# Kernel optimization log

Hardware: AMD Instinct MI355X
Metric: run time of the kernel (lower is better)

## Reference

```python
import jax, jax.numpy as jnp
import numpy as np

OUT_K = 7  # out_kernel


def setup_inputs() -> dict:
    key = jax.random.key(0)
    k = jax.random.split(key, 12)
    b, cin, h, w = 2, 256, 64, 64
    C, pd = 64, 4          # out_channels, pos_dim
    qc = C - pd            # channels produced by conv_q/k/v
    s = 0.05
    f32 = jnp.float32
    return {
        "x":    jax.random.normal(k[0], (b, cin, h, w), f32),
        "Wq":   jax.random.normal(k[1], (qc, cin), f32) * s,
        "bq":   jax.random.normal(k[2], (qc,), f32) * s,
        "Wk":   jax.random.normal(k[3], (qc, cin), f32) * s,
        "bk":   jax.random.normal(k[4], (qc,), f32) * s,
        "Wv":   jax.random.normal(k[5], (qc, cin), f32) * s,
        "bv":   jax.random.normal(k[6], (qc,), f32) * s,
        "Wp":   jax.random.normal(k[7], (pd, 2), f32) * s,
        "bp":   jax.random.normal(k[8], (pd,), f32) * s,
        "Wout": jax.random.normal(k[9], (C, C, OUT_K, OUT_K), f32) * s,
        "bout": jax.random.normal(k[10], (C,), f32) * s,
    }


def reference(x, Wq, bq, Wk, bk, Wv, bv, Wp, bp, Wout, bout):
    b, cin, h, w = x.shape
    C = Wout.shape[0]  # out_channels
    dt = x.dtype

    # positional encoding: hw_pose is (row_index, col_index) grids -> 1x1 conv to pos_dim chans
    rows = jnp.broadcast_to(jnp.arange(h, dtype=dt)[:, None], (h, w))
    cols = jnp.broadcast_to(jnp.arange(w, dtype=dt)[None, :], (h, w))
    grid = jnp.stack([rows, cols], axis=0)                      # (2,h,w)
    pos = jnp.einsum('oc,chw->ohw', Wp, grid) + bp[:, None, None]  # (pd,h,w)
    pos = jnp.broadcast_to(pos[None], (b,) + pos.shape)         # (b,pd,h,w)

    def conv1x1(W, bias):
        return jnp.einsum('bchw,oc->bohw', x, W) + bias[None, :, None, None]

    qs = jnp.concatenate([conv1x1(Wq, bq), pos], axis=1)        # (b,C,h,w)
    ks = jnp.concatenate([conv1x1(Wk, bk), pos], axis=1)
    vs = jnp.concatenate([conv1x1(Wv, bv), pos], axis=1)

    hw = h * w
    qsf = qs.transpose(0, 2, 3, 1).reshape(b, hw, C)            # (b,hw,C)
    ksf = ks.reshape(b, C, hw)                                  # (b,C,hw)
    vsf = vs.transpose(0, 2, 3, 1)                              # (b,h,w,C)

    qk = jnp.einsum('bnc,bcm->bnm', qsf, ksf) / jnp.sqrt(jnp.asarray(C, dt))
    diag = jnp.arange(hw)
    qk = qk.at[:, diag, diag].set(0.0)                          # zero diagonal BEFORE softmax
    attn = jax.nn.softmax(qk, axis=-1).reshape(b, h, w, h, w)

    # 7x7 clamped neighborhood gather (replaces the 49-iteration python loop)
    r = OUT_K // 2
    offs = jnp.arange(-r, r + 1)
    hi = jnp.clip(jnp.arange(h)[:, None] + offs[None, :], 0, h - 1)  # (h,7)
    wi = jnp.clip(jnp.arange(w)[:, None] + offs[None, :], 0, w - 1)  # (w,7)
    ii = jnp.arange(h)[:, None, None, None]
    jj = jnp.arange(w)[None, :, None, None]
    hk = hi[:, None, :, None]
    wk = wi[None, :, None, :]
    attn_loc = attn[:, ii, jj, hk, wk]                          # (b,h,w,7,7)
    v_loc = vsf[:, hk, wk, :]                                   # (b,h,w,7,7,C)

    qkv = attn_loc[..., None] * v_loc                           # (b,h,w,7,7,C)
    # con_out: kernel=7, stride=7 over a 7x7 patch == full contraction
    out = jnp.einsum('bhwklc,ockl->bhwo', qkv, Wout) + bout     # (b,h,w,C)
    out = jax.nn.relu(out)
    return out.transpose(0, 3, 1, 2)                            # (b,C,h,w)
```

## Files before the change

### kernel.cpp

```cpp
#include <hip/hip_runtime.h>
#include <math.h>

#define NTAP 49

typedef short bf16x8 __attribute__((ext_vector_type(8)));
typedef float f32x4  __attribute__((ext_vector_type(4)));

__device__ __forceinline__ float b2f(ushort u) {
    return __uint_as_float(((unsigned)u) << 16);
}
__device__ __forceinline__ ushort f2b(float f) {
    unsigned u = __float_as_uint(f);
    return (ushort)((u + 0x7FFFu + ((u >> 16) & 1u)) >> 16);
}
__device__ __forceinline__ int iclamp(int x) { return min(max(x, 0), 63); }

#define LOG2E 1.44269504f
#define S2    (0.125f * LOG2E)

#define WTB_OFF 0u
#define QH_OFF  598016u
#define KH_OFF  1646592u
#define VH_OFF  2695168u
#define LP_OFF  3743744u
#define MXQ_OFF 4005888u
#define MXK_OFF 4006912u

__device__ __forceinline__ float mh_reduce(const float* __restrict__ MXq,
                                           const float* __restrict__ MXk,
                                           int b, int t, float* sh) {
    if (t < 64) {
        float a = fmaxf(MXq[(b << 7) + t], MXq[(b << 7) + 64 + t]);
        float k = fmaxf(MXk[(b << 7) + t], MXk[(b << 7) + 64 + t]);
        #pragma unroll
        for (int off = 1; off < 64; off <<= 1) {
            a = fmaxf(a, __shfl_xor(a, off, 64));
            k = fmaxf(k, __shfl_xor(k, off, 64));
        }
        if (t == 0) *sh = 0.125f * sqrtf(a) * sqrtf(k) + 1.0f;
    }
    __syncthreads();
    return *sh;
}

__global__ __launch_bounds__(512, 2) void k_qkv(
    const float* __restrict__ x,
    const float* __restrict__ Wq, const float* __restrict__ Wk, const float* __restrict__ Wv,
    const float* __restrict__ bq, const float* __restrict__ bk, const float* __restrict__ bv,
    const float* __restrict__ Wp, const float* __restrict__ bp,
    ushort* __restrict__ QKV, float* __restrict__ MXq, float* __restrict__ MXk)
{
    __shared__ ushort Xh[32 * 256];
    __shared__ ushort Xl[32 * 256];
    __shared__ ushort Wshl[192 * 64];
    __shared__ float  sqL[64];
    int bid0 = blockIdx.x;
    int bid  = (bid0 & 7) * 32 + (bid0 >> 3);
    int b   = bid >> 7;
    int n0  = (bid & 127) * 32;
    int t   = threadIdx.x;
    int w    = t >> 6;
    int L    = t & 63;
    int lrow = L & 15, lk = L >> 4;

    if (t < 64) sqL[t] = 0.f;
    {
        int p  = t & 31;
        int cg = t >> 5;
        #pragma unroll
        for (int it = 0; it < 2; ++it) {
            int cgi = cg + it * 16;
            float v[8];
            #pragma unroll
            for (int e = 0; e < 8; ++e)
                v[e] = x[((size_t)(b * 256 + cgi * 8 + e) << 12) + n0 + p];
            bf16x8 hi, lo;
            #pragma unroll
            for (int e = 0; e < 8; ++e) {
                ushort h = f2b(v[e]);
                hi[e] = (short)h;
                lo[e] = (short)f2b(v[e] - b2f(h));
            }
            int off = p * 256 + ((cgi * 8) ^ ((p & 7) * 8));
            *(bf16x8*)(Xh + off) = hi;
            *(bf16x8*)(Xl + off) = lo;
        }
    }

    int   s_och[3], s_g[3];
    bool  s_live[3];
    const float* s_src[3];
    #pragma unroll
    for (int s = 0; s < 3; ++s) {
        int g_idx = t + s * 512;
        int och = g_idx >> 3, g = g_idx & 7;
        int mat = och >> 6, o = och & 63;
        const float* Wm = (mat == 0) ? Wq : (mat == 1) ? Wk : Wv;
        s_och[s] = och; s_g[s] = g;
        s_live[s] = (o < 60);
        s_src[s] = Wm + o * 256 + (g & 3) * 8;
    }
    float4 wreg[3][2];

    #define ISSUE_W(c8) {                                                   \
        _Pragma("unroll")                                                   \
        for (int s = 0; s < 3; ++s) {                                       \
            if (s_live[s]) {                                                \
                const float* sp = s_src[s] + (c8) * 32;                     \
                wreg[s][0] = *(const float4*)(sp);                          \
                wreg[s][1] = *(const float4*)(sp + 4);                      \
            } else {                                                        \
                wreg[s][0] = make_float4(0.f,0.f,0.f,0.f);                  \
                wreg[s][1] = make_float4(0.f,0.f,0.f,0.f);                  \
            }                                                               \
        } }
    #define WRITE_W() {                                                     \
        _Pragma("unroll")                                                   \
        for (int s = 0; s < 3; ++s) {                                       \
            float vv[8] = {wreg[s][0].x, wreg[s][0].y, wreg[s][0].z,        \
                           wreg[s][0].w, wreg[s][1].x, wreg[s][1].y,        \
                           wreg[s][1].z, wreg[s][1].w};                     \
            bf16x8 val;                                                     \
            _Pragma("unroll")                                               \
            for (int e = 0; e < 8; ++e) {                                   \
                ushort h = f2b(vv[e]);                                      \
                val[e] = (s_g[s] < 4) ? (short)h                            \
                                      : (short)f2b(vv[e] - b2f(h));         \
            }                                                               \
            *(bf16x8*)((char*)Wshl + s_och[s] * 128 +                       \
                       ((s_g[s] * 16) ^ ((s_och[s] & 7) << 4))) = val;      \
        } }

    ISSUE_W(0);
    __syncthreads();
    WRITE_W();
    __syncthreads();

    int pxh = w >> 2;
    int ob  = (w & 3) * 48;
    int px  = pxh * 16 + lrow;

    f32x4 acc[3] = {{0,0,0,0},{0,0,0,0},{0,0,0,0}};

    for (int c8 = 0; c8 < 8; ++c8) {
        if (c8 + 1 < 8) ISSUE_W(c8 + 1);
        int cidx = (c8 * 4 + lk) * 8;
        int o0 = px * 256 + (cidx ^ ((px & 7) * 8));
        bf16x8 ah = *(const bf16x8*)(Xh + o0);
        bf16x8 al = *(const bf16x8*)(Xl + o0);
        __builtin_amdgcn_s_setprio(1);
        #pragma unroll
        for (int c = 0; c < 3; ++c) {
            int och = ob + c * 16 + lrow;
            const char* wb = (const char*)Wshl + och * 128;
            int swz = (och & 7) << 4;
            bf16x8 bh = *(const bf16x8*)(wb + ((lk * 16) ^ swz));
            bf16x8 bl = *(const bf16x8*)(wb + (((4 + lk) * 16) ^ swz));
            acc[c] = __builtin_amdgcn_mfma_f32_16x16x32_bf16(al, bh, acc[c], 0, 0, 0);
            acc[c] = __builtin_amdgcn_mfma_f32_16x16x32_bf16(ah, bl, acc[c], 0, 0, 0);
            acc[c] = __builtin_amdgcn_mfma_f32_16x16x32_bf16(ah, bh, acc[c], 0, 0, 0);
        }
        __builtin_amdgcn_s_setprio(0);
        __syncthreads();
        if (c8 + 1 < 8) WRITE_W();
        __syncthreads();
    }

    float s_q[4] = {0,0,0,0}, s_k[4] = {0,0,0,0};
    #pragma unroll
    for (int c = 0; c < 3; ++c) {
        int och = ob + c * 16 + lrow;
        int mat = och >> 6;
        int o   = och & 63;
        const float* bm = (mat == 0) ? bq : (mat == 1) ? bk : bv;
        ushort* Ob = QKV + (size_t)mat * 524288;
        if (o < 60) {
            float bias = bm[o];
            #pragma unroll
            for (int e = 0; e < 4; ++e) {
                int n = n0 + pxh * 16 + lk * 4 + e;
                float v = acc[c][e] + bias;
                Ob[((size_t)((b << 12) + n)) * 64 + o] = f2b(v);
                if (mat == 0) s_q[e] = fmaf(v, v, s_q[e]);
                else if (mat == 1) s_k[e] = fmaf(v, v, s_k[e]);
            }
        } else {
            int po = o - 60;
            float w0 = Wp[2 * po], w1 = Wp[2 * po + 1], b0 = bp[po];
            #pragma unroll
            for (int e = 0; e < 4; ++e) {
                int n = n0 + pxh * 16 + lk * 4 + e;
                float fi = (float)(n >> 6), fj = (float)(n & 63);
                float pv = fmaf(w0, fi, fmaf(w1, fj, b0));
                Ob[((size_t)((b << 12) + n)) * 64 + o] = f2b(pv);
                if (mat == 0) s_q[e] = fmaf(pv, pv, s_q[e]);
                else if (mat == 1) s_k[e] = fmaf(pv, pv, s_k[e]);
            }
        }
    }
    #pragma unroll
    for (int off = 1; off < 16; off <<= 1) {
        #pragma unroll
        for (int e = 0; e < 4; ++e) {
            s_q[e] += __shfl_xor(s_q[e], off, 64);
            s_k[e] += __shfl_xor(s_k[e], off, 64);
        }
    }
    if (lrow == 0) {
        #pragma unroll
        for (int e = 0; e < 4; ++e) {
            int pix = pxh * 16 + lk * 4 + e;
            atomicAdd(&sqL[pix],      s_q[e]);
            atomicAdd(&sqL[32 + pix], s_k[e]);
        }
    }
    __syncthreads();
    if (t < 32) {
        float q2 = sqL[t], k2 = sqL[32 + t];
        #pragma unroll
        for (int off = 1; off < 32; off <<= 1) {
            q2 = fmaxf(q2, __shfl_xor(q2, off, 64));
            k2 = fmaxf(k2, __shfl_xor(k2, off, 64));
        }
        if (t == 0) { MXq[bid] = q2; MXk[bid] = k2; }
    }
}

__global__ __launch_bounds__(512, 2) void k_stats(
    const float* __restrict__ Wout, ushort* __restrict__ Wtb,
    const ushort* __restrict__ QH, const ushort* __restrict__ KH,
    const float* __restrict__ MXq, const float* __restrict__ MXk,
    float* __restrict__ Lp)
{
    __shared__ ushort Ks[2][128 * 64];
    __shared__ float  mhs;
    int bid0 = blockIdx.x;
    int bid  = (bid0 & 7) * 64 + (bid0 >> 3);
    int ks  = bid & 7;
    int r   = bid >> 3;
    int b   = r >> 5;
    int n0  = (r & 31) * 128;
    int ck0 = ks * 512;
    int t = threadIdx.x;

    {
        int widx = bid * 512 + t;
        if (widx < 64 * 64 * NTAP) {
            int o   = widx / (64 * NTAP);
            int rem = widx - o * (64 * NTAP);
            int c   = rem / NTAP;
            int kl  = rem - c * NTAP;
            Wtb[(o * NTAP + kl) * 64 + c] = f2b(Wout[widx]);
        }
    }
    float bse = -mh_reduce(MXq, MXk, b, t, &mhs) * LOG2E;

    int w = t >> 6, L = t & 63;
    int lrow = L & 15, lk = L >> 4;

    size_t qbase = ((size_t)((b << 12) + n0 + w * 16 + lrow)) * 64 + lk * 8;
    bf16x8 a0 = *(const bf16x8*)(QH + qbase);
    bf16x8 a1 = *(const bf16x8*)(QH + qbase + 32);

    #pragma unroll
    for (int gi = 0; gi < 2; ++gi) {
        int g = t + gi * 512;
        int u = g >> 3, c8 = g & 7;
        bf16x8 val = *(const bf16x8*)(KH + ((size_t)((b << 12) + ck0 + u)) * 64 + c8 * 8);
        *(bf16x8*)((char*)Ks[0] + u * 128 + ((c8 * 16) ^ ((u & 7) << 4))) = val;
    }

    float rs0 = 0.f, rs1 = 0.f, rs2 = 0.f, rs3 = 0.f;

    for (int c = 0; c < 4; ++c) {
        bf16x8 st0, st1;
        int u0 = t >> 3, c80 = t & 7;
        int u1 = (t + 512) >> 3, c81 = t & 7;
        bool pf = (c + 1) < 4;
        if (pf) {
            st0 = *(const bf16x8*)(KH + ((size_t)((b << 12) + ck0 + (c + 1) * 128 + u0)) * 64 + c80 * 8);
            st1 = *(const bf16x8*)(KH + ((size_t)((b << 12) + ck0 + (c + 1) * 128 + u1)) * 64 + c81 * 8);
        }
        __syncthreads();
        const char* kb = (const char*)Ks[c & 1];
        __builtin_amdgcn_s_setprio(1);
        #pragma unroll
        for (int kg = 0; kg < 8; ++kg) {
            int u = kg * 16 + lrow;
            int swz = (u & 7) << 4;
            bf16x8 b0 = *(const bf16x8*)(kb + u * 128 + ((lk * 16) ^ swz));
            bf16x8 b1 = *(const bf16x8*)(kb + u * 128 + ((64 + lk * 16) ^ swz));
            f32x4 z = {0.f, 0.f, 0.f, 0.f};
            z = __builtin_amdgcn_mfma_f32_16x16x32_bf16(a0, b0, z, 0, 0, 0);
            z = __builtin_amdgcn_mfma_f32_16x16x32_bf16(a1, b1, z, 0, 0, 0);
            rs0 += exp2f(fmaf(z[0], S2, bse));
            rs1 += exp2f(fmaf(z[1], S2, bse));
            rs2 += exp2f(fmaf(z[2], S2, bse));
            rs3 += exp2f(fmaf(z[3], S2, bse));
        }
        __builtin_amdgcn_s_setprio(0);
        if (pf) {
            char* kn = (char*)Ks[(c + 1) & 1];
            *(bf16x8*)(kn + u0 * 128 + ((c80 * 16) ^ ((u0 & 7) << 4))) = st0;
            *(bf16x8*)(kn + u1 * 128 + ((c81 * 16) ^ ((u1 & 7) << 4))) = st1;
        }
    }
    #pragma unroll
    for (int off = 1; off < 16; off <<= 1) {
        rs0 += __shfl_xor(rs0, off, 64);
        rs1 += __shfl_xor(rs1, off, 64);
        rs2 += __shfl_xor(rs2, off, 64);
        rs3 += __shfl_xor(rs3, off, 64);
    }
    if (lrow == 0) {
        float* dst = Lp + ((size_t)(ks * 2 + b) << 12) + n0 + w * 16 + lk * 4;
        dst[0] = rs0; dst[1] = rs1; dst[2] = rs2; dst[3] = rs3;
    }
}

__global__ __launch_bounds__(512, 1) void k_out(
    const ushort* __restrict__ QH, const ushort* __restrict__ KH,
    const ushort* __restrict__ VH, const ushort* __restrict__ Wtb,
    const float* __restrict__ Lp,
    const float* __restrict__ MXq, const float* __restrict__ MXk,
    const float* __restrict__ bout, float* __restrict__ out)
{
    __shared__ ushort Vs[7 * 40 * 64];
    __shared__ ushort Kh[7 * 40 * 64];
    __shared__ ushort Ws[7 * 64 * 64];
    __shared__ float  Al2[NTAP * 36];
    __shared__ float  Lrow[32];
    __shared__ float  LcS[32];
    __shared__ float  mhs;
    int bid0 = blockIdx.x;
    int bid  = (bid0 & 7) * 32 + (bid0 >> 3);
    int b   = bid >> 7;
    int rem = bid & 127;
    int i   = rem >> 1;
    int j0  = (rem & 1) * 32;
    int n0  = (i << 6) + j0;
    int t   = threadIdx.x;
    int w    = t >> 6;
    int L    = t & 63;
    int lrow = L & 15, lk = L >> 4;

    float bse = -mh_reduce(MXq, MXk, b, t, &mhs) * LOG2E;
    float e0  = exp2f(bse);

    bf16x8 wreg[7];
    #define ISSUE_WS(kk) {                                                          \
        _Pragma("unroll")                                                           \
        for (int s = 0; s < 7; ++s) {                                               \
            int g = t + s * 512;                                                    \
            int c8 = g & 7, och = (g >> 3) & 63, ll = g >> 9;                       \
            wreg[s] = *(const bf16x8*)(Wtb + ((size_t)(och * NTAP + (kk) * 7 + ll)) * 64 + c8 * 8); \
        } }
    #define WRITE_WS() {                                                            \
        _Pragma("unroll")                                                           \
        for (int s = 0; s < 7; ++s) {                                               \
            int g = t + s * 512;                                                    \
            int c8 = g & 7, och = (g >> 3) & 63, ll = g >> 9;                       \
            *(bf16x8*)((char*)Ws + ll * 8192 + och * 128 +                          \
                       ((c8 * 16) ^ ((och & 7) << 4))) = wreg[s];                   \
        } }

    for (int g = t; g < 2 * 7 * 38 * 8; g += 512) {
        int which = g >= 7 * 38 * 8;
        int gg = which ? g - 7 * 38 * 8 : g;
        int kk = gg / 304;
        int r2 = gg - kk * 304;
        int u  = r2 >> 3, c8 = r2 & 7;
        int vr = iclamp(i + kk - 3);
        int vc = iclamp(j0 - 3 + u);
        const ushort* src = which ? KH : VH;
        ushort* dst = which ? Kh : Vs;
        bf16x8 val = *(const bf16x8*)(src + ((size_t)((b << 12) + (vr << 6) + vc)) * 64 + c8 * 8);
        *(bf16x8*)((char*)dst + kk * 5120 + u * 128 + ((c8 * 16) ^ ((u & 7) << 4))) = val;
    }
    ISSUE_WS(0);
    WRITE_WS();
    if (t < 32) {
        int n = n0 + t;
        float s = 0.f;
        #pragma unroll
        for (int ks = 0; ks < 8; ++ks)
            s += Lp[((size_t)(ks * 2 + b) << 12) + n];
        Lrow[t] = s;
    }
    __syncthreads();

    {
        int p = t >> 4, u = t & 15;
        int n = n0 + p;
        int pj = n & 63;
        const ushort* qr = QH + ((size_t)(b << 12) + n) * 64;
        bf16x8 qv[8];
        #pragma unroll
        for (int c8 = 0; c8 < 8; ++c8) qv[c8] = *(const bf16x8*)(qr + c8 * 8);

        int nt = (u == 0) ? 4 : 3;
        float d[4] = {0.f, 0.f, 0.f, 0.f};
        int srcs[4];
        const char* kbp[4];
        int swzs[4];
        #pragma unroll
        for (int m = 0; m < 4; ++m) {
            int tap = (m == 3) ? 48 : (u + 16 * m);
            int kk = tap / 7, ll = tap - kk * 7;
            srcs[m] = (iclamp(i + kk - 3) << 6) + iclamp(pj + ll - 3);
            int uu = p + ll;
            kbp[m]  = (const char*)Kh + kk * 5120 + uu * 128;
            swzs[m] = (uu & 7) << 4;
        }
        #pragma unroll
        for (int c8 = 0; c8 < 8; ++c8) {
            bf16x8 kv0 = *(const bf16x8*)(kbp[0] + ((c8 * 16) ^ swzs[0]));
            bf16x8 kv1 = *(const bf16x8*)(kbp[1] + ((c8 * 16) ^ swzs[1]));
            bf16x8 kv2 = *(const bf16x8*)(kbp[2] + ((c8 * 16) ^ swzs[2]));
            #pragma unroll
            for (int e = 0; e < 8; ++e) {
                float q = b2f((ushort)qv[c8][e]);
                d[0] = fmaf(q, b2f((ushort)kv0[e]), d[0]);
                d[1] = fmaf(q, b2f((ushort)kv1[e]), d[1]);
                d[2] = fmaf(q, b2f((ushort)kv2[e]), d[2]);
            }
        }
        if (nt == 4) {
            #pragma unroll
            for (int c8 = 0; c8 < 8; ++c8) {
                bf16x8 kv3 = *(const bf16x8*)(kbp[3] + ((c8 * 16) ^ swzs[3]));
                #pragma unroll
                for (int e = 0; e < 8; ++e)
                    d[3] = fmaf(b2f((ushort)qv[c8][e]), b2f((ushort)kv3[e]), d[3]);
            }
        }
        if (u == 8)
            LcS[p] = Lrow[p] - exp2f(fmaf(d[1], S2, bse)) + e0;
        __syncthreads();
        float rLc = 1.0f / LcS[p];
        for (int m = 0; m < nt; ++m) {
            int tap = (m == 3) ? 48 : (u + 16 * m);
            float A = (srcs[m] == n) ? (e0 * rLc)
                                     : (exp2f(fmaf(d[m], S2, bse)) * rLc);
            Al2[tap * 36 + p] = A;
        }
    }
    __syncthreads();

    int q16 = (w >> 2) << 4;
    int o16 = (w & 3) << 4;
    int oA  = o16 + lrow;
    int wswz = (oA & 7) << 4;
    f32x4 acc0 = {0.f, 0.f, 0.f, 0.f};

    for (int kk = 0; kk < 7; ++kk) {
        if (kk + 1 < 7) ISSUE_WS(kk + 1);
        const char* vrow = (const char*)Vs + kk * 5120;
        __builtin_amdgcn_s_setprio(1);
        #pragma unroll
        for (int ll = 0; ll < 7; ++ll) {
            int kl = kk * 7 + ll;
            int u = q16 + lrow + ll;
            const char* vb = vrow + u * 128;
            int swz = (u & 7) << 4;
            bf16x8 v0 = *(const bf16x8*)(vb + ((lk * 16) ^ swz));
            bf16x8 v1 = *(const bf16x8*)(vb + ((64 + lk * 16) ^ swz));
            float4 av = *(const float4*)(&Al2[kl * 36 + q16 + lk * 4]);
            const char* wb = (const char*)Ws + ll * 8192 + oA * 128;
            bf16x8 b00 = *(const bf16x8*)(wb + ((lk * 16) ^ wswz));
            bf16x8 b01 = *(const bf16x8*)(wb + (((4 + lk) * 16) ^ wswz));
            f32x4 z = {0.f, 0.f, 0.f, 0.f};
            z = __builtin_amdgcn_mfma_f32_16x16x32_bf16(v0, b00, z, 0, 0, 0);
            z = __builtin_amdgcn_mfma_f32_16x16x32_bf16(v1, b01, z, 0, 0, 0);
            acc0[0] = fmaf(av.x, z[0], acc0[0]);
            acc0[1] = fmaf(av.y, z[1], acc0[1]);
            acc0[2] = fmaf(av.z, z[2], acc0[2]);
            acc0[3] = fmaf(av.w, z[3], acc0[3]);
        }
        __builtin_amdgcn_s_setprio(0);
        __syncthreads();
        if (kk + 1 < 7) WRITE_WS();
        __syncthreads();
    }

    int o = oA;
    int nbase = n0 + q16 + lk * 4;
    float bb = bout[o];
    float4 v = make_float4(fmaxf(acc0[0] + bb, 0.f), fmaxf(acc0[1] + bb, 0.f),
                           fmaxf(acc0[2] + bb, 0.f), fmaxf(acc0[3] + bb, 0.f));
    *(float4*)(out + (((size_t)(b * 64 + o)) << 12) + nbase) = v;
}

extern "C" void kernel_launch(void* const* d_in, const int* in_sizes, int n_in,
                              void* d_out, int out_size, void* d_ws, size_t ws_size,
                              hipStream_t stream) {
    const float* x    = (const float*)d_in[0];
    const float* Wq   = (const float*)d_in[1];
    const float* bq   = (const float*)d_in[2];
    const float* Wk   = (const float*)d_in[3];
    const float* bk   = (const float*)d_in[4];
    const float* Wv   = (const float*)d_in[5];
    const float* bv   = (const float*)d_in[6];
    const float* Wp   = (const float*)d_in[7];
    const float* bp   = (const float*)d_in[8];
    const float* Wout = (const float*)d_in[9];
    const float* bout = (const float*)d_in[10];
    float* out = (float*)d_out;

    char* ws = (char*)d_ws;
    ushort* Wtb = (ushort*)(ws + WTB_OFF);
    ushort* QKV = (ushort*)(ws + QH_OFF);
    float*  Lp  = (float*)(ws + LP_OFF);
    float*  MXq = (float*)(ws + MXQ_OFF);
    float*  MXk = (float*)(ws + MXK_OFF);

    ushort* QH = QKV;
    ushort* KH = QKV + 524288;
    ushort* VH = QKV + 1048576;

    hipLaunchKernelGGL(k_qkv,   dim3(256), dim3(512), 0, stream,
                       x, Wq, Wk, Wv, bq, bk, bv, Wp, bp, QKV, MXq, MXk);
    hipLaunchKernelGGL(k_stats, dim3(512), dim3(512), 0, stream,
                       Wout, Wtb, QH, KH, MXq, MXk, Lp);
    hipLaunchKernelGGL(k_out,   dim3(256), dim3(512), 0, stream,
                       QH, KH, VH, Wtb, Lp, MXq, MXk, bout, out);
}
```

Baseline: 46.13 us.

## Double-buffer output-conv weight tiles in LDS, aliasing second buffer over K halo

Replaces the separate shared arrays with one manually laid-out LDS buffer so the 7x64x64 weight slice can be double-buffered. The second weight buffer reuses the K-halo region, which is dead after the attention-weight phase. With two buffers, the barrier before writing the next weight slice is dropped, leaving one barrier per kk iteration instead of two. The cost is a larger LDS footprint (about 157 KB) and reliance on the K region being unused by the time it is overwritten.

```diff
diff --git a/kernel.cpp b/kernel.cpp
--- a/kernel.cpp
+++ b/kernel.cpp
@@ -318,6 +318,14 @@
     }
 }
 
+#define SM_VS   0
+#define SM_WS0  35840
+#define SM_WS1  93184
+#define SM_KHA  93184
+#define SM_AL2  150528
+#define SM_LROW 157584
+#define SM_LCS  157712
+#define SM_MHS  157840
 __global__ __launch_bounds__(512, 1) void k_out(
     const ushort* __restrict__ QH, const ushort* __restrict__ KH,
     const ushort* __restrict__ VH, const ushort* __restrict__ Wtb,
@@ -325,13 +333,13 @@
     const float* __restrict__ MXq, const float* __restrict__ MXk,
     const float* __restrict__ bout, float* __restrict__ out)
 {
-    __shared__ ushort Vs[7 * 40 * 64];
-    __shared__ ushort Kh[7 * 40 * 64];
-    __shared__ ushort Ws[7 * 64 * 64];
-    __shared__ float  Al2[NTAP * 36];
-    __shared__ float  Lrow[32];
-    __shared__ float  LcS[32];
-    __shared__ float  mhs;
+    __shared__ __align__(16) char smem[157856];
+    char*  Vsb  = smem + SM_VS;
+    char*  Khb  = smem + SM_KHA;
+    float* Al2  = (float*)(smem + SM_AL2);
+    float* Lrow = (float*)(smem + SM_LROW);
+    float* LcS  = (float*)(smem + SM_LCS);
+
     int bid0 = blockIdx.x;
     int bid  = (bid0 & 7) * 32 + (bid0 >> 3);
     int b   = bid >> 7;
@@ -344,7 +352,7 @@
     int L    = t & 63;
     int lrow = L & 15, lk = L >> 4;
 
-    float bse = -mh_reduce(MXq, MXk, b, t, &mhs) * LOG2E;
+    float bse = -mh_reduce(MXq, MXk, b, t, (float*)(smem + SM_MHS)) * LOG2E;
     float e0  = exp2f(bse);
 
     bf16x8 wreg[7];
@@ -355,12 +363,12 @@
             int c8 = g & 7, och = (g >> 3) & 63, ll = g >> 9;                       \
             wreg[s] = *(const bf16x8*)(Wtb + ((size_t)(och * NTAP + (kk) * 7 + ll)) * 64 + c8 * 8); \
         } }
-    #define WRITE_WS() {                                                            \
+    #define WRITE_WS(dstb) {                                                        \
         _Pragma("unroll")                                                           \
         for (int s = 0; s < 7; ++s) {                                               \
             int g = t + s * 512;                                                    \
             int c8 = g & 7, och = (g >> 3) & 63, ll = g >> 9;                       \
-            *(bf16x8*)((char*)Ws + ll * 8192 + och * 128 +                          \
+            *(bf16x8*)((dstb) + ll * 8192 + och * 128 +                             \
                        ((c8 * 16) ^ ((och & 7) << 4))) = wreg[s];                   \
         } }
 
@@ -373,12 +381,12 @@
         int vr = iclamp(i + kk - 3);
         int vc = iclamp(j0 - 3 + u);
         const ushort* src = which ? KH : VH;
-        ushort* dst = which ? Kh : Vs;
+        char* dst = which ? Khb : Vsb;
         bf16x8 val = *(const bf16x8*)(src + ((size_t)((b << 12) + (vr << 6) + vc)) * 64 + c8 * 8);
-        *(bf16x8*)((char*)dst + kk * 5120 + u * 128 + ((c8 * 16) ^ ((u & 7) << 4))) = val;
+        *(bf16x8*)(dst + kk * 5120 + u * 128 + ((c8 * 16) ^ ((u & 7) << 4))) = val;
     }
     ISSUE_WS(0);
-    WRITE_WS();
+    WRITE_WS(smem + SM_WS0);
     if (t < 32) {
         int n = n0 + t;
         float s = 0.f;
@@ -409,7 +417,7 @@
             int kk = tap / 7, ll = tap - kk * 7;
             srcs[m] = (iclamp(i + kk - 3) << 6) + iclamp(pj + ll - 3);
             int uu = p + ll;
-            kbp[m]  = (const char*)Kh + kk * 5120 + uu * 128;
+            kbp[m]  = Khb + kk * 5120 + uu * 128;
             swzs[m] = (uu & 7) << 4;
         }
         #pragma unroll
@@ -455,7 +463,8 @@
 
     for (int kk = 0; kk < 7; ++kk) {
         if (kk + 1 < 7) ISSUE_WS(kk + 1);
-        const char* vrow = (const char*)Vs + kk * 5120;
+        const char* vrow = Vsb + kk * 5120;
+        const char* wsb  = smem + ((kk & 1) ? SM_WS1 : SM_WS0);
         __builtin_amdgcn_s_setprio(1);
         #pragma unroll
         for (int ll = 0; ll < 7; ++ll) {
@@ -466,7 +475,7 @@
             bf16x8 v0 = *(const bf16x8*)(vb + ((lk * 16) ^ swz));
             bf16x8 v1 = *(const bf16x8*)(vb + ((64 + lk * 16) ^ swz));
             float4 av = *(const float4*)(&Al2[kl * 36 + q16 + lk * 4]);
-            const char* wb = (const char*)Ws + ll * 8192 + oA * 128;
+            const char* wb = wsb + ll * 8192 + oA * 128;
             bf16x8 b00 = *(const bf16x8*)(wb + ((lk * 16) ^ wswz));
             bf16x8 b01 = *(const bf16x8*)(wb + (((4 + lk) * 16) ^ wswz));
             f32x4 z = {0.f, 0.f, 0.f, 0.f};
@@ -478,8 +487,7 @@
             acc0[3] = fmaf(av.w, z[3], acc0[3]);
         }
         __builtin_amdgcn_s_setprio(0);
-        __syncthreads();
-        if (kk + 1 < 7) WRITE_WS();
+        if (kk + 1 < 7) WRITE_WS(smem + (((kk + 1) & 1) ? SM_WS1 : SM_WS0));
         __syncthreads();
     }
 
```

Measured after the change: 45.40 us (median of 2 runs). About the same (-1.6%).
